# Kernel tuning notes

Measured on AMD Instinct MI355X. Metric: run time of the kernel, lower is better.

The kernel has to match this reference:

```python
import jax, jax.numpy as jnp
import numpy as np

N_NODES = 100000


def gcn_conv(x, src, dst, w, W, b, n):
    """PyG GCNConv: out = D^{-1/2} (A+I) D^{-1/2} (x @ W) + b (self-loops weight 1)."""
    loop = jnp.arange(n, dtype=src.dtype)
    s = jnp.concatenate([src, loop])
    d = jnp.concatenate([dst, loop])
    ew = jnp.concatenate([w, jnp.ones((n,), x.dtype)])
    deg = jax.ops.segment_sum(ew, d, num_segments=n)            # degree of target nodes
    dinv = jnp.where(deg > 0, jax.lax.rsqrt(deg), jnp.zeros_like(deg))
    norm = dinv[s] * ew * dinv[d]                               # [E+N]
    h = x @ W                                                   # [N, out] dense transform first
    msg = h[s] * norm[:, None]                                  # gather + scale
    out = jax.ops.segment_sum(msg, d, num_segments=n)           # scatter-add aggregate
    return out + b


def setup_inputs() -> dict:
    key = jax.random.key(0)
    k1, k2, k3, k4, k5, k6 = jax.random.split(key, 6)
    in_dim, hid, out_dim = 128, 128, 64
    n_edges = 1600000
    x = jax.random.normal(k1, (N_NODES, in_dim), dtype=jnp.float32)
    edge_index = jax.random.randint(k2, (2, n_edges), 0, N_NODES, dtype=jnp.int32)
    edge_weight = jax.random.uniform(k3, (n_edges,), dtype=jnp.float32)
    # Glorot-style weights, zero bias (as in GCNConv defaults)
    W1 = jax.random.normal(k4, (in_dim, hid), dtype=jnp.float32) / np.sqrt(in_dim)
    b1 = jnp.zeros((hid,), jnp.float32)
    W2 = jax.random.normal(k5, (hid, out_dim), dtype=jnp.float32) / np.sqrt(hid)
    b2 = jnp.zeros((out_dim,), jnp.float32)
    return {"x": x, "edge_index": edge_index, "edge_weight": edge_weight,
            "W1": W1, "b1": b1, "W2": W2, "b2": b2}


def reference(x, edge_index, edge_weight, W1, b1, W2, b2):
    src, dst = edge_index[0], edge_index[1]
    h = gcn_conv(x, src, dst, edge_weight, W1, b1, N_NODES)
    h = jax.nn.relu(h)
    # dropout is identity in eval mode
    out = gcn_conv(h, src, dst, edge_weight, W2, b2, N_NODES)
    return out
```

## Files before the change

### kernel.cpp

```cpp
#include <hip/hip_runtime.h>
#include <cstdint>
#include <cstddef>


typedef unsigned long long u64;
typedef unsigned int u32;
typedef unsigned short u16;

__device__ __forceinline__ float bflo(u32 u) { return __uint_as_float(u << 16); }
__device__ __forceinline__ float bfhi(u32 u) { return __uint_as_float(u & 0xffff0000u); }
__device__ __forceinline__ u32 f2bf(float f) {
  u32 u = __float_as_uint(f);
  return (u + 0x7fffu + ((u >> 16) & 1u)) >> 16;
}
__device__ __forceinline__ u32 pack2bf(float lo, float hi) {
  return f2bf(lo) | (f2bf(hi) << 16);
}

__global__ void init_kernel(u64* packed, int n) {
  int i = blockIdx.x * 256 + threadIdx.x;
  if (i < n) packed[i] = (1ull << 32);
}

__global__ void degrank_kernel(const int* __restrict__ dst, const float* __restrict__ w,
                               u64* packed, u16* __restrict__ rank, int E) {
  int e = blockIdx.x * 256 + threadIdx.x;
  if (e < E) {
    int d = dst[e];
    u64 add = (1ull << 48) | (u64)(w[e] * 4294967296.0f);
    u64 old = atomicAdd(&packed[d], add);
    rank[e] = (u16)(old >> 48);
  }
}

__global__ __launch_bounds__(256) void gemm1_kernel(const float* __restrict__ x,
                                                    const float* __restrict__ W1,
                                                    u16* __restrict__ h1, int M) {
  __shared__ float As[128][64];
  __shared__ float Ws[128][64];
  const int tid = threadIdx.x;
  const int tx = tid & 15;
  const int ty = tid >> 4;
  const int rowbase = blockIdx.x * 64;
  const int colbase = blockIdx.y * 64;

  for (int i = tid; i < 64 * 32; i += 256) {
    int row = i & 63;
    int k4 = (i >> 6) << 2;
    int gr = rowbase + row;
    float4 v = make_float4(0.f, 0.f, 0.f, 0.f);
    if (gr < M) v = *reinterpret_cast<const float4*>(x + (size_t)gr * 128 + k4);
    As[k4 + 0][row] = v.x;
    As[k4 + 1][row] = v.y;
    As[k4 + 2][row] = v.z;
    As[k4 + 3][row] = v.w;
  }
  for (int i = tid; i < 128 * 16; i += 256) {
    int c4 = (i & 15) << 2;
    int k = i >> 4;
    float4 v = *reinterpret_cast<const float4*>(W1 + (size_t)k * 128 + colbase + c4);
    *reinterpret_cast<float4*>(&Ws[k][c4]) = v;
  }
  __syncthreads();

  float acc[4][4] = {};
  #pragma unroll 8
  for (int k = 0; k < 128; ++k) {
    float4 a = *reinterpret_cast<const float4*>(&As[k][ty << 2]);
    float4 b = *reinterpret_cast<const float4*>(&Ws[k][tx << 2]);
    acc[0][0] += a.x * b.x; acc[0][1] += a.x * b.y; acc[0][2] += a.x * b.z; acc[0][3] += a.x * b.w;
    acc[1][0] += a.y * b.x; acc[1][1] += a.y * b.y; acc[1][2] += a.y * b.z; acc[1][3] += a.y * b.w;
    acc[2][0] += a.z * b.x; acc[2][1] += a.z * b.y; acc[2][2] += a.z * b.z; acc[2][3] += a.z * b.w;
    acc[3][0] += a.w * b.x; acc[3][1] += a.w * b.y; acc[3][2] += a.w * b.z; acc[3][3] += a.w * b.w;
  }
  #pragma unroll
  for (int r = 0; r < 4; ++r) {
    int gr = rowbase + (ty << 2) + r;
    if (gr < M) {
      uint2 p;
      p.x = pack2bf(acc[r][0], acc[r][1]);
      p.y = pack2bf(acc[r][2], acc[r][3]);
      *reinterpret_cast<uint2*>(h1 + (size_t)gr * 128 + colbase + (tx << 2)) = p;
    }
  }
}

__global__ void scan1_kernel(const u64* __restrict__ packed, int* __restrict__ rowstart,
                             int* __restrict__ bsum, float* __restrict__ dinvp, int n) {
  __shared__ int wsum[4];
  int b = blockIdx.x;
  int base = b * 1024;
  int tid = threadIdx.x;
  int lane = tid & 63, wv = tid >> 6;
  int idx = base + tid * 4;
  int v0 = 0, v1 = 0, v2 = 0, v3 = 0;
  #pragma unroll
  for (int j = 0; j < 4; ++j) {
    if (idx + j < n) {
      u64 p = packed[idx + j];
      int c = (int)(p >> 48);
      if (j == 0) v0 = c; else if (j == 1) v1 = c; else if (j == 2) v2 = c; else v3 = c;
      float deg = (float)((double)(p & 0xFFFFFFFFFFFFull) * 2.3283064365386963e-10);
      dinvp[idx + j] = rsqrtf(deg);
    }
  }
  int tsum = v0 + v1 + v2 + v3;
  int inc = tsum;
  #pragma unroll
  for (int off = 1; off < 64; off <<= 1) {
    int u = __shfl_up(inc, off, 64);
    if (lane >= off) inc += u;
  }
  if (lane == 63) wsum[wv] = inc;
  __syncthreads();
  int woff = 0;
  for (int w2 = 0; w2 < wv; ++w2) woff += wsum[w2];
  int texc = woff + inc - tsum;
  if (idx     < n) rowstart[idx]     = texc;
  if (idx + 1 < n) rowstart[idx + 1] = texc + v0;
  if (idx + 2 < n) rowstart[idx + 2] = texc + v0 + v1;
  if (idx + 3 < n) rowstart[idx + 3] = texc + v0 + v1 + v2;
  if (tid == 255) {
    bsum[b] = woff + inc;
    if (b == (int)gridDim.x - 1) rowstart[n] = woff + inc;
  }
}

__global__ void scan2_kernel(const int* __restrict__ bsum, int* __restrict__ boff, int nblk) {
  __shared__ int wsum[4];
  int tid = threadIdx.x, lane = tid & 63, wv = tid >> 6;
  int v = (tid < nblk) ? bsum[tid] : 0;
  int inc = v;
  #pragma unroll
  for (int off = 1; off < 64; off <<= 1) {
    int u = __shfl_up(inc, off, 64);
    if (lane >= off) inc += u;
  }
  if (lane == 63) wsum[wv] = inc;
  __syncthreads();
  int woff = 0;
  for (int w2 = 0; w2 < wv; ++w2) woff += wsum[w2];
  if (tid < nblk) boff[tid] = woff + inc - v;
}

__global__ void fill_kernel(const int* __restrict__ src, const int* __restrict__ dst,
                            const float* __restrict__ w, const u16* __restrict__ rank,
                            const float* __restrict__ dinv, const int* __restrict__ rowstart,
                            const int* __restrict__ boff, int2* __restrict__ erec, int E) {
  int e = blockIdx.x * 256 + threadIdx.x;
  if (e < E) {
    int s = src[e], d = dst[e];
    int pos = rowstart[d] + boff[d >> 10] + (int)rank[e];
    float nrm = dinv[s] * w[e] * dinv[d];
    erec[pos] = make_int2(s, __float_as_int(nrm));
  }
}

__global__ __launch_bounds__(256) void gemm2_kernel(const u16* __restrict__ A,
                                                    const float* __restrict__ W,
                                                    u16* __restrict__ C, int M) {
  __shared__ float As[128][64];
  __shared__ float Ws[128][64];
  const int tid = threadIdx.x;
  const int tx = tid & 15;
  const int ty = tid >> 4;
  const int rowbase = blockIdx.x * 64;

  for (int i = tid; i < 64 * 32; i += 256) {
    int row = i & 63;
    int chunk = i >> 6;
    int k4 = chunk << 2;
    int gr = rowbase + row;
    float f0 = 0.f, f1 = 0.f, f2 = 0.f, f3 = 0.f;
    if (gr < M) {
      uint2 u = reinterpret_cast<const uint2*>(A + (size_t)gr * 128)[chunk];
      f0 = bflo(u.x); f1 = bfhi(u.x); f2 = bflo(u.y); f3 = bfhi(u.y);
    }
    As[k4 + 0][row] = f0;
    As[k4 + 1][row] = f1;
    As[k4 + 2][row] = f2;
    As[k4 + 3][row] = f3;
  }
  for (int i = tid; i < 128 * 16; i += 256) {
    int c4 = (i & 15) << 2;
    int k = i >> 4;
    float4 v = *reinterpret_cast<const float4*>(W + (size_t)k * 64 + c4);
    *reinterpret_cast<float4*>(&Ws[k][c4]) = v;
  }
  __syncthreads();

  float acc[4][4] = {};
  #pragma unroll 8
  for (int k = 0; k < 128; ++k) {
    float4 a = *reinterpret_cast<const float4*>(&As[k][ty << 2]);
    float4 b = *reinterpret_cast<const float4*>(&Ws[k][tx << 2]);
    acc[0][0] += a.x * b.x; acc[0][1] += a.x * b.y; acc[0][2] += a.x * b.z; acc[0][3] += a.x * b.w;
    acc[1][0] += a.y * b.x; acc[1][1] += a.y * b.y; acc[1][2] += a.y * b.z; acc[1][3] += a.y * b.w;
    acc[2][0] += a.z * b.x; acc[2][1] += a.z * b.y; acc[2][2] += a.z * b.z; acc[2][3] += a.z * b.w;
    acc[3][0] += a.w * b.x; acc[3][1] += a.w * b.y; acc[3][2] += a.w * b.z; acc[3][3] += a.w * b.w;
  }
  #pragma unroll
  for (int r = 0; r < 4; ++r) {
    int gr = rowbase + (ty << 2) + r;
    if (gr < M) {
      uint2 p;
      p.x = pack2bf(acc[r][0], acc[r][1]);
      p.y = pack2bf(acc[r][2], acc[r][3]);
      *reinterpret_cast<uint2*>(C + (size_t)gr * 64 + (tx << 2)) = p;
    }
  }
}

__global__ __launch_bounds__(256) void agg128_relu_kernel(
    const u32* __restrict__ H, const int* __restrict__ rowstart,
    const int* __restrict__ boff, const int2* __restrict__ erec,
    const float* __restrict__ dinv, const float* __restrict__ bias,
    u32* __restrict__ out, int n) {
  int wid = (blockIdx.x * 256 + threadIdx.x) >> 6;
  int lane = threadIdx.x & 63;
  if (wid >= n) return;
  float dv = dinv[wid];
  float ns = dv * dv;
  u32 hv = H[(size_t)wid * 64 + lane];
  float a0 = ns * bflo(hv), a1 = ns * bfhi(hv);
  int e0 = rowstart[wid] + boff[wid >> 10];
  int e1 = rowstart[wid + 1] + boff[(wid + 1) >> 10];
  int e = e0;
  for (; e + 3 < e1; e += 4) {
    int2 r0 = erec[e], r1 = erec[e + 1], r2 = erec[e + 2], r3 = erec[e + 3];
    u32 v0 = H[(size_t)r0.x * 64 + lane];
    u32 v1 = H[(size_t)r1.x * 64 + lane];
    u32 v2 = H[(size_t)r2.x * 64 + lane];
    u32 v3 = H[(size_t)r3.x * 64 + lane];
    float w0 = __int_as_float(r0.y), w1 = __int_as_float(r1.y);
    float w2 = __int_as_float(r2.y), w3 = __int_as_float(r3.y);
    a0 += w0 * bflo(v0) + w1 * bflo(v1) + w2 * bflo(v2) + w3 * bflo(v3);
    a1 += w0 * bfhi(v0) + w1 * bfhi(v1) + w2 * bfhi(v2) + w3 * bfhi(v3);
  }
  for (; e < e1; ++e) {
    int2 r = erec[e];
    u32 v = H[(size_t)r.x * 64 + lane];
    float w = __int_as_float(r.y);
    a0 += w * bflo(v);
    a1 += w * bfhi(v);
  }
  float2 bb = reinterpret_cast<const float2*>(bias)[lane];
  a0 = fmaxf(a0 + bb.x, 0.f);
  a1 = fmaxf(a1 + bb.y, 0.f);
  out[(size_t)wid * 64 + lane] = pack2bf(a0, a1);
}

__global__ __launch_bounds__(256) void agg64_kernel(
    const u16* __restrict__ H, const int* __restrict__ rowstart,
    const int* __restrict__ boff, const int2* __restrict__ erec,
    const float* __restrict__ dinv, const float* __restrict__ bias,
    float* __restrict__ out, int n) {
  int wid = (blockIdx.x * 256 + threadIdx.x) >> 6;
  int lane = threadIdx.x & 63;
  if (wid >= n) return;
  float dv = dinv[wid];
  float ns = dv * dv;
  float a0 = ns * bflo((u32)H[(size_t)wid * 64 + lane]);
  int e0 = rowstart[wid] + boff[wid >> 10];
  int e1 = rowstart[wid + 1] + boff[(wid + 1) >> 10];
  int e = e0;
  for (; e + 3 < e1; e += 4) {
    int2 r0 = erec[e], r1 = erec[e + 1], r2 = erec[e + 2], r3 = erec[e + 3];
    float v0 = bflo((u32)H[(size_t)r0.x * 64 + lane]);
    float v1 = bflo((u32)H[(size_t)r1.x * 64 + lane]);
    float v2 = bflo((u32)H[(size_t)r2.x * 64 + lane]);
    float v3 = bflo((u32)H[(size_t)r3.x * 64 + lane]);
    a0 += __int_as_float(r0.y) * v0 + __int_as_float(r1.y) * v1 +
          __int_as_float(r2.y) * v2 + __int_as_float(r3.y) * v3;
  }
  for (; e < e1; ++e) {
    int2 r = erec[e];
    a0 += __int_as_float(r.y) * bflo((u32)H[(size_t)r.x * 64 + lane]);
  }
  out[(size_t)wid * 64 + lane] = a0 + bias[lane];
}

extern "C" void kernel_launch(void* const* d_in, const int* in_sizes, int n_in,
                              void* d_out, int out_size, void* d_ws, size_t ws_size,
                              hipStream_t stream) {
  const float* x  = (const float*)d_in[0];
  const int*   ei = (const int*)d_in[1];
  const float* ew = (const float*)d_in[2];
  const float* W1 = (const float*)d_in[3];
  const float* b1 = (const float*)d_in[4];
  const float* W2 = (const float*)d_in[5];
  const float* b2 = (const float*)d_in[6];
  float* out = (float*)d_out;
  const int N = in_sizes[0] / 128;
  const int E = in_sizes[2];
  const int* src = ei;
  const int* dst = ei + E;

  char* wsB = (char*)d_ws;
  size_t off = 0;
  auto alloc = [&](size_t bytes) {
    void* p = wsB + off;
    off += ((bytes + 255) / 256) * 256;
    return p;
  };
  u64*   packed = (u64*)alloc((size_t)N * 8);
  float* dinv   = (float*)alloc((size_t)N * 4);
  u16*   rank   = (u16*)alloc((size_t)E * 2);
  int*   rowst  = (int*)alloc((size_t)(N + 1) * 4);
  int*   bsum   = (int*)alloc(256 * 4);
  int*   boff   = (int*)alloc(256 * 4);
  int2*  erec   = (int2*)alloc((size_t)E * 8);
  u16*   h1     = (u16*)alloc((size_t)N * 128 * 2);
  u16*   a1     = (u16*)alloc((size_t)N * 128 * 2);
  u16*   h2     = h1;

  const int nb = (N + 255) / 256;
  const int eb = (E + 255) / 256;
  const int nbx = (N + 63) / 64;
  const int nblk = (N + 1023) / 1024;

  init_kernel<<<nb, 256, 0, stream>>>(packed, N);
  degrank_kernel<<<eb, 256, 0, stream>>>(dst, ew, packed, rank, E);
  dim3 g1(nbx, 2);
  gemm1_kernel<<<g1, 256, 0, stream>>>(x, W1, h1, N);
  scan1_kernel<<<nblk, 256, 0, stream>>>(packed, rowst, bsum, dinv, N);
  scan2_kernel<<<1, 256, 0, stream>>>(bsum, boff, nblk);
  fill_kernel<<<eb, 256, 0, stream>>>(src, dst, ew, rank, dinv, rowst, boff, erec, E);

  const int ab = (N + 3) / 4;
  agg128_relu_kernel<<<ab, 256, 0, stream>>>((const u32*)h1, rowst, boff, erec, dinv, b1,
                                             (u32*)a1, N);
  gemm2_kernel<<<nbx, 256, 0, stream>>>(a1, W2, h2, N);
  agg64_kernel<<<ab, 256, 0, stream>>>(h2, rowst, boff, erec, dinv, b2, out, N);
}
```

Before: 472.7 us.

## Use bf16 MFMA for both GEMMs and process two nodes per wave in aggregation

Both dense transforms now run on MFMA 16x16x32 bf16 instructions. The first GEMM splits the fp32 input into hi/lo bf16 parts to keep accuracy, and the weights are transposed into shared memory as bf16. The aggregation kernels assign half a wavefront per node with wider per-lane loads (uint2 or u32), so 32 lanes cover a row instead of 64 and each lane does more work per gathered edge. This is meant to cut GEMM compute time and raise memory-level parallelism in the gather. In exchange, W1 and W2 are rounded to bf16 inside the GEMMs, and every block recomputes the weight transpose.

```diff
diff --git a/kernel.cpp b/kernel.cpp
--- a/kernel.cpp
+++ b/kernel.cpp
@@ -6,6 +6,8 @@
 typedef unsigned long long u64;
 typedef unsigned int u32;
 typedef unsigned short u16;
+typedef __attribute__((ext_vector_type(8))) short bf16x8;
+typedef __attribute__((ext_vector_type(4))) float f32x4;
 
 __device__ __forceinline__ float bflo(u32 u) { return __uint_as_float(u << 16); }
 __device__ __forceinline__ float bfhi(u32 u) { return __uint_as_float(u & 0xffff0000u); }
@@ -36,51 +38,57 @@
 __global__ __launch_bounds__(256) void gemm1_kernel(const float* __restrict__ x,
                                                     const float* __restrict__ W1,
                                                     u16* __restrict__ h1, int M) {
-  __shared__ float As[128][64];
-  __shared__ float Ws[128][64];
+  __shared__ u16 Wt[128][136];
   const int tid = threadIdx.x;
-  const int tx = tid & 15;
-  const int ty = tid >> 4;
-  const int rowbase = blockIdx.x * 64;
-  const int colbase = blockIdx.y * 64;
-
-  for (int i = tid; i < 64 * 32; i += 256) {
-    int row = i & 63;
-    int k4 = (i >> 6) << 2;
-    int gr = rowbase + row;
-    float4 v = make_float4(0.f, 0.f, 0.f, 0.f);
-    if (gr < M) v = *reinterpret_cast<const float4*>(x + (size_t)gr * 128 + k4);
-    As[k4 + 0][row] = v.x;
-    As[k4 + 1][row] = v.y;
-    As[k4 + 2][row] = v.z;
-    As[k4 + 3][row] = v.w;
-  }
-  for (int i = tid; i < 128 * 16; i += 256) {
-    int c4 = (i & 15) << 2;
-    int k = i >> 4;
-    float4 v = *reinterpret_cast<const float4*>(W1 + (size_t)k * 128 + colbase + c4);
-    *reinterpret_cast<float4*>(&Ws[k][c4]) = v;
+  for (int i = tid; i < 128 * 128; i += 256) {
+    int c = i >> 7, k = i & 127;
+    Wt[c][k] = (u16)f2bf(W1[(size_t)k * 128 + c]);
   }
   __syncthreads();
 
-  float acc[4][4] = {};
-  #pragma unroll 8
-  for (int k = 0; k < 128; ++k) {
-    float4 a = *reinterpret_cast<const float4*>(&As[k][ty << 2]);
-    float4 b = *reinterpret_cast<const float4*>(&Ws[k][tx << 2]);
-    acc[0][0] += a.x * b.x; acc[0][1] += a.x * b.y; acc[0][2] += a.x * b.z; acc[0][3] += a.x * b.w;
-    acc[1][0] += a.y * b.x; acc[1][1] += a.y * b.y; acc[1][2] += a.y * b.z; acc[1][3] += a.y * b.w;
-    acc[2][0] += a.z * b.x; acc[2][1] += a.z * b.y; acc[2][2] += a.z * b.z; acc[2][3] += a.z * b.w;
-    acc[3][0] += a.w * b.x; acc[3][1] += a.w * b.y; acc[3][2] += a.w * b.z; acc[3][3] += a.w * b.w;
-  }
-  #pragma unroll
-  for (int r = 0; r < 4; ++r) {
-    int gr = rowbase + (ty << 2) + r;
-    if (gr < M) {
-      uint2 p;
-      p.x = pack2bf(acc[r][0], acc[r][1]);
-      p.y = pack2bf(acc[r][2], acc[r][3]);
-      *reinterpret_cast<uint2*>(h1 + (size_t)gr * 128 + colbase + (tx << 2)) = p;
+  const int wv = tid >> 6;
+  const int l = tid & 63;
+  const int c16 = l & 15;
+  const int kg = l >> 4;
+  const int arow = blockIdx.x * 64 + wv * 16 + c16;
+  const bool rok = arow < M;
+
+  bf16x8 ahi[4], alo[4];
+  #pragma unroll
+  for (int kk = 0; kk < 4; ++kk) {
+    float v[8];
+    if (rok) {
+      float4 p0 = *reinterpret_cast<const float4*>(x + (size_t)arow * 128 + kk * 32 + kg * 8);
+      float4 p1 = *reinterpret_cast<const float4*>(x + (size_t)arow * 128 + kk * 32 + kg * 8 + 4);
+      v[0] = p0.x; v[1] = p0.y; v[2] = p0.z; v[3] = p0.w;
+      v[4] = p1.x; v[5] = p1.y; v[6] = p1.z; v[7] = p1.w;
+    } else {
+      #pragma unroll
+      for (int j = 0; j < 8; ++j) v[j] = 0.f;
+    }
+    #pragma unroll
+    for (int j = 0; j < 8; ++j) {
+      u32 hb = f2bf(v[j]);
+      float hf = __uint_as_float(hb << 16);
+      u32 lb = f2bf(v[j] - hf);
+      ahi[kk][j] = (short)hb;
+      alo[kk][j] = (short)lb;
+    }
+  }
+
+  #pragma unroll
+  for (int ct = 0; ct < 8; ++ct) {
+    f32x4 acc = {0.f, 0.f, 0.f, 0.f};
+    #pragma unroll
+    for (int kk = 0; kk < 4; ++kk) {
+      bf16x8 b = *reinterpret_cast<const bf16x8*>(&Wt[ct * 16 + c16][kk * 32 + kg * 8]);
+      acc = __builtin_amdgcn_mfma_f32_16x16x32_bf16(alo[kk], b, acc, 0, 0, 0);
+      acc = __builtin_amdgcn_mfma_f32_16x16x32_bf16(ahi[kk], b, acc, 0, 0, 0);
+    }
+    #pragma unroll
+    for (int r = 0; r < 4; ++r) {
+      int gr = blockIdx.x * 64 + wv * 16 + kg * 4 + r;
+      if (gr < M) h1[(size_t)gr * 128 + ct * 16 + c16] = (u16)f2bf(acc[r]);
     }
   }
 }
@@ -157,127 +165,130 @@
 }
 
 __global__ __launch_bounds__(256) void gemm2_kernel(const u16* __restrict__ A,
-                                                    const float* __restrict__ W,
+                                                    const float* __restrict__ W2,
                                                     u16* __restrict__ C, int M) {
-  __shared__ float As[128][64];
-  __shared__ float Ws[128][64];
+  __shared__ u16 Wt[64][136];
   const int tid = threadIdx.x;
-  const int tx = tid & 15;
-  const int ty = tid >> 4;
-  const int rowbase = blockIdx.x * 64;
-
-  for (int i = tid; i < 64 * 32; i += 256) {
-    int row = i & 63;
-    int chunk = i >> 6;
-    int k4 = chunk << 2;
-    int gr = rowbase + row;
-    float f0 = 0.f, f1 = 0.f, f2 = 0.f, f3 = 0.f;
-    if (gr < M) {
-      uint2 u = reinterpret_cast<const uint2*>(A + (size_t)gr * 128)[chunk];
-      f0 = bflo(u.x); f1 = bfhi(u.x); f2 = bflo(u.y); f3 = bfhi(u.y);
-    }
-    As[k4 + 0][row] = f0;
-    As[k4 + 1][row] = f1;
-    As[k4 + 2][row] = f2;
-    As[k4 + 3][row] = f3;
-  }
-  for (int i = tid; i < 128 * 16; i += 256) {
-    int c4 = (i & 15) << 2;
-    int k = i >> 4;
-    float4 v = *reinterpret_cast<const float4*>(W + (size_t)k * 64 + c4);
-    *reinterpret_cast<float4*>(&Ws[k][c4]) = v;
+  for (int i = tid; i < 128 * 64; i += 256) {
+    int c = i >> 7, k = i & 127;
+    Wt[c][k] = (u16)f2bf(W2[(size_t)k * 64 + c]);
   }
   __syncthreads();
 
-  float acc[4][4] = {};
-  #pragma unroll 8
-  for (int k = 0; k < 128; ++k) {
-    float4 a = *reinterpret_cast<const float4*>(&As[k][ty << 2]);
-    float4 b = *reinterpret_cast<const float4*>(&Ws[k][tx << 2]);
-    acc[0][0] += a.x * b.x; acc[0][1] += a.x * b.y; acc[0][2] += a.x * b.z; acc[0][3] += a.x * b.w;
-    acc[1][0] += a.y * b.x; acc[1][1] += a.y * b.y; acc[1][2] += a.y * b.z; acc[1][3] += a.y * b.w;
-    acc[2][0] += a.z * b.x; acc[2][1] += a.z * b.y; acc[2][2] += a.z * b.z; acc[2][3] += a.z * b.w;
-    acc[3][0] += a.w * b.x; acc[3][1] += a.w * b.y; acc[3][2] += a.w * b.z; acc[3][3] += a.w * b.w;
-  }
-  #pragma unroll
-  for (int r = 0; r < 4; ++r) {
-    int gr = rowbase + (ty << 2) + r;
-    if (gr < M) {
-      uint2 p;
-      p.x = pack2bf(acc[r][0], acc[r][1]);
-      p.y = pack2bf(acc[r][2], acc[r][3]);
-      *reinterpret_cast<uint2*>(C + (size_t)gr * 64 + (tx << 2)) = p;
+  const int wv = tid >> 6;
+  const int l = tid & 63;
+  const int c16 = l & 15;
+  const int kg = l >> 4;
+  const int arow = blockIdx.x * 64 + wv * 16 + c16;
+  const bool rok = arow < M;
+
+  bf16x8 af[4];
+  #pragma unroll
+  for (int kk = 0; kk < 4; ++kk) {
+    if (rok) {
+      af[kk] = *reinterpret_cast<const bf16x8*>(A + (size_t)arow * 128 + kk * 32 + kg * 8);
+    } else {
+      af[kk] = bf16x8{0, 0, 0, 0, 0, 0, 0, 0};
+    }
+  }
+
+  #pragma unroll
+  for (int ct = 0; ct < 4; ++ct) {
+    f32x4 acc = {0.f, 0.f, 0.f, 0.f};
+    #pragma unroll
+    for (int kk = 0; kk < 4; ++kk) {
+      bf16x8 b = *reinterpret_cast<const bf16x8*>(&Wt[ct * 16 + c16][kk * 32 + kg * 8]);
+      acc = __builtin_amdgcn_mfma_f32_16x16x32_bf16(af[kk], b, acc, 0, 0, 0);
+    }
+    #pragma unroll
+    for (int r = 0; r < 4; ++r) {
+      int gr = blockIdx.x * 64 + wv * 16 + kg * 4 + r;
+      if (gr < M) C[(size_t)gr * 64 + ct * 16 + c16] = (u16)f2bf(acc[r]);
     }
   }
 }
 
 __global__ __launch_bounds__(256) void agg128_relu_kernel(
+    const uint2* __restrict__ H2, const int* __restrict__ rowstart,
+    const int* __restrict__ boff, const int2* __restrict__ erec,
+    const float* __restrict__ dinv, const float* __restrict__ bias,
+    uint2* __restrict__ out2, int n) {
+  int wid = (blockIdx.x * 256 + threadIdx.x) >> 6;
+  int lane = threadIdx.x & 63;
+  int node = wid * 2 + (lane >> 5);
+  int hl = lane & 31;
+  if (node >= n) return;
+  float dv = dinv[node];
+  float ns = dv * dv;
+  uint2 hv = H2[(size_t)node * 32 + hl];
+  float a0 = ns * bflo(hv.x), a1 = ns * bfhi(hv.x);
+  float a2 = ns * bflo(hv.y), a3 = ns * bfhi(hv.y);
+  int e  = rowstart[node] + boff[node >> 10];
+  int e1 = rowstart[node + 1] + boff[(node + 1) >> 10];
+  for (; e + 3 < e1; e += 4) {
+    int2 r0 = erec[e], r1 = erec[e + 1], r2 = erec[e + 2], r3 = erec[e + 3];
+    uint2 v0 = H2[(size_t)r0.x * 32 + hl];
+    uint2 v1 = H2[(size_t)r1.x * 32 + hl];
+    uint2 v2 = H2[(size_t)r2.x * 32 + hl];
+    uint2 v3 = H2[(size_t)r3.x * 32 + hl];
+    float w0 = __int_as_float(r0.y), w1 = __int_as_float(r1.y);
+    float w2 = __int_as_float(r2.y), w3 = __int_as_float(r3.y);
+    a0 += w0 * bflo(v0.x) + w1 * bflo(v1.x) + w2 * bflo(v2.x) + w3 * bflo(v3.x);
+    a1 += w0 * bfhi(v0.x) + w1 * bfhi(v1.x) + w2 * bfhi(v2.x) + w3 * bfhi(v3.x);
+    a2 += w0 * bflo(v0.y) + w1 * bflo(v1.y) + w2 * bflo(v2.y) + w3 * bflo(v3.y);
+    a3 += w0 * bfhi(v0.y) + w1 * bfhi(v1.y) + w2 * bfhi(v2.y) + w3 * bfhi(v3.y);
+  }
+  for (; e < e1; ++e) {
+    int2 r = erec[e];
+    uint2 v = H2[(size_t)r.x * 32 + hl];
+    float w = __int_as_float(r.y);
+    a0 += w * bflo(v.x); a1 += w * bfhi(v.x);
+    a2 += w * bflo(v.y); a3 += w * bfhi(v.y);
+  }
+  float4 bb = reinterpret_cast<const float4*>(bias)[hl];
+  a0 = fmaxf(a0 + bb.x, 0.f);
+  a1 = fmaxf(a1 + bb.y, 0.f);
+  a2 = fmaxf(a2 + bb.z, 0.f);
+  a3 = fmaxf(a3 + bb.w, 0.f);
+  out2[(size_t)node * 32 + hl] = make_uint2(pack2bf(a0, a1), pack2bf(a2, a3));
+}
+
+__global__ __launch_bounds__(256) void agg64_kernel(
     const u32* __restrict__ H, const int* __restrict__ rowstart,
     const int* __restrict__ boff, const int2* __restrict__ erec,
     const float* __restrict__ dinv, const float* __restrict__ bias,
-    u32* __restrict__ out, int n) {
+    float2* __restrict__ out2, int n) {
   int wid = (blockIdx.x * 256 + threadIdx.x) >> 6;
   int lane = threadIdx.x & 63;
-  if (wid >= n) return;
-  float dv = dinv[wid];
+  int node = wid * 2 + (lane >> 5);
+  int hl = lane & 31;
+  if (node >= n) return;
+  float dv = dinv[node];
   float ns = dv * dv;
-  u32 hv = H[(size_t)wid * 64 + lane];
+  u32 hv = H[(size_t)node * 32 + hl];
   float a0 = ns * bflo(hv), a1 = ns * bfhi(hv);
-  int e0 = rowstart[wid] + boff[wid >> 10];
-  int e1 = rowstart[wid + 1] + boff[(wid + 1) >> 10];
-  int e = e0;
+  int e  = rowstart[node] + boff[node >> 10];
+  int e1 = rowstart[node + 1] + boff[(node + 1) >> 10];
   for (; e + 3 < e1; e += 4) {
     int2 r0 = erec[e], r1 = erec[e + 1], r2 = erec[e + 2], r3 = erec[e + 3];
-    u32 v0 = H[(size_t)r0.x * 64 + lane];
-    u32 v1 = H[(size_t)r1.x * 64 + lane];
-    u32 v2 = H[(size_t)r2.x * 64 + lane];
-    u32 v3 = H[(size_t)r3.x * 64 + lane];
-    float w0 = __int_as_float(r0.y), w1 = __int_as_float(r1.y);
-    float w2 = __int_as_float(r2.y), w3 = __int_as_float(r3.y);
-    a0 += w0 * bflo(v0) + w1 * bflo(v1) + w2 * bflo(v2) + w3 * bflo(v3);
-    a1 += w0 * bfhi(v0) + w1 * bfhi(v1) + w2 * bfhi(v2) + w3 * bfhi(v3);
+    u32 v0 = H[(size_t)r0.x * 32 + hl];
+    u32 v1 = H[(size_t)r1.x * 32 + hl];
+    u32 v2 = H[(size_t)r2.x * 32 + hl];
+    u32 v3 = H[(size_t)r3.x * 32 + hl];
+    a0 += __int_as_float(r0.y) * bflo(v0) + __int_as_float(r1.y) * bflo(v1)
+        + __int_as_float(r2.y) * bflo(v2) + __int_as_float(r3.y) * bflo(v3);
+    a1 += __int_as_float(r0.y) * bfhi(v0) + __int_as_float(r1.y) * bfhi(v1)
+        + __int_as_float(r2.y) * bfhi(v2) + __int_as_float(r3.y) * bfhi(v3);
   }
   for (; e < e1; ++e) {
     int2 r = erec[e];
-    u32 v = H[(size_t)r.x * 64 + lane];
+    u32 v = H[(size_t)r.x * 32 + hl];
     float w = __int_as_float(r.y);
     a0 += w * bflo(v);
     a1 += w * bfhi(v);
   }
-  float2 bb = reinterpret_cast<const float2*>(bias)[lane];
-  a0 = fmaxf(a0 + bb.x, 0.f);
-  a1 = fmaxf(a1 + bb.y, 0.f);
-  out[(size_t)wid * 64 + lane] = pack2bf(a0, a1);
-}
-
-__global__ __launch_bounds__(256) void agg64_kernel(
-    const u16* __restrict__ H, const int* __restrict__ rowstart,
-    const int* __restrict__ boff, const int2* __restrict__ erec,
-    const float* __restrict__ dinv, const float* __restrict__ bias,
-    float* __restrict__ out, int n) {
-  int wid = (blockIdx.x * 256 + threadIdx.x) >> 6;
-  int lane = threadIdx.x & 63;
-  if (wid >= n) return;
-  float dv = dinv[wid];
-  float ns = dv * dv;
-  float a0 = ns * bflo((u32)H[(size_t)wid * 64 + lane]);
-  int e0 = rowstart[wid] + boff[wid >> 10];
-  int e1 = rowstart[wid + 1] + boff[(wid + 1) >> 10];
-  int e = e0;
-  for (; e + 3 < e1; e += 4) {
-    int2 r0 = erec[e], r1 = erec[e + 1], r2 = erec[e + 2], r3 = erec[e + 3];
-    float v0 = bflo((u32)H[(size_t)r0.x * 64 + lane]);
-    float v1 = bflo((u32)H[(size_t)r1.x * 64 + lane]);
-    float v2 = bflo((u32)H[(size_t)r2.x * 64 + lane]);
-    float v3 = bflo((u32)H[(size_t)r3.x * 64 + lane]);
-    a0 += __int_as_float(r0.y) * v0 + __int_as_float(r1.y) * v1 +
-          __int_as_float(r2.y) * v2 + __int_as_float(r3.y) * v3;
-  }
-  for (; e < e1; ++e) {
-    int2 r = erec[e];
-    a0 += __int_as_float(r.y) * bflo((u32)H[(size_t)r.x * 64 + lane]);
-  }
-  out[(size_t)wid * 64 + lane] = a0 + bias[lane];
+  float2 bb = reinterpret_cast<const float2*>(bias)[hl];
+  out2[(size_t)node * 32 + hl] = make_float2(a0 + bb.x, a1 + bb.y);
 }
 
 extern "C" void kernel_launch(void* const* d_in, const int* in_sizes, int n_in,
@@ -321,15 +332,15 @@
 
   init_kernel<<<nb, 256, 0, stream>>>(packed, N);
   degrank_kernel<<<eb, 256, 0, stream>>>(dst, ew, packed, rank, E);
-  dim3 g1(nbx, 2);
-  gemm1_kernel<<<g1, 256, 0, stream>>>(x, W1, h1, N);
+  gemm1_kernel<<<nbx, 256, 0, stream>>>(x, W1, h1, N);
   scan1_kernel<<<nblk, 256, 0, stream>>>(packed, rowst, bsum, dinv, N);
   scan2_kernel<<<1, 256, 0, stream>>>(bsum, boff, nblk);
   fill_kernel<<<eb, 256, 0, stream>>>(src, dst, ew, rank, dinv, rowst, boff, erec, E);
 
-  const int ab = (N + 3) / 4;
-  agg128_relu_kernel<<<ab, 256, 0, stream>>>((const u32*)h1, rowst, boff, erec, dinv, b1,
-                                             (u32*)a1, N);
+  const int ab = (N + 7) / 8;
+  agg128_relu_kernel<<<ab, 256, 0, stream>>>((const uint2*)h1, rowst, boff, erec, dinv, b1,
+                                             (uint2*)a1, N);
   gemm2_kernel<<<nbx, 256, 0, stream>>>(a1, W2, h2, N);
-  agg64_kernel<<<ab, 256, 0, stream>>>(h2, rowst, boff, erec, dinv, b2, out, N);
-}
+  agg64_kernel<<<ab, 256, 0, stream>>>((const u32*)h2, rowst, boff, erec, dinv, b2,
+                                       (float2*)out, N);
+}
```

Result: faster. 432.1 us (-8.6%).
